# Kernel tuning notes

Hardware: AMD Instinct MI355X
Metric: run time of the kernel (lower is better)

Reference implementation:

```python
import jax, jax.numpy as jnp
import numpy as np

DECAY = 0.95     # importance_decay
BUDGET = 1.0     # attention_budget
TOP_K = 10       # recall top_k used by get_context_embedding
EPS = 1e-8


def _gelu(x):
    # torch nn.GELU default = exact erf variant
    return jax.nn.gelu(x, approximate=False)


def setup_inputs() -> dict:
    key = jax.random.key(0)
    ks = jax.random.split(key, 8)
    B, N, D, H = 4096, 100, 4096, 128
    query = jax.random.normal(ks[0], (B, D), dtype=jnp.float32)
    seg_emb = jax.random.normal(ks[1], (N, D), dtype=jnp.float32)
    positions = jnp.arange(N, dtype=jnp.int32)
    s1 = 1.0 / np.sqrt(D)
    s2 = 1.0 / np.sqrt(H)
    iw1 = jax.random.normal(ks[2], (D, H), dtype=jnp.float32) * s1
    ib1 = jnp.zeros((H,), dtype=jnp.float32)
    iw2 = jax.random.normal(ks[3], (H, 1), dtype=jnp.float32) * s2
    ib2 = jnp.zeros((1,), dtype=jnp.float32)
    rw1 = jax.random.normal(ks[4], (2 * D, H), dtype=jnp.float32) * (1.0 / np.sqrt(2 * D))
    rb1 = jnp.zeros((H,), dtype=jnp.float32)
    rw2 = jax.random.normal(ks[5], (H, 1), dtype=jnp.float32) * s2
    rb2 = jnp.zeros((1,), dtype=jnp.float32)
    return {"query": query, "seg_emb": seg_emb, "positions": positions,
            "iw1": iw1, "ib1": ib1, "iw2": iw2, "ib2": ib2,
            "rw1": rw1, "rb1": rb1, "rw2": rw2, "rb2": rb2}


def reference(query, seg_emb, positions, iw1, ib1, iw2, ib2, rw1, rb1, rw2, rb2):
    # query: [B, D], seg_emb: [N, D]
    B, D = query.shape
    N = seg_emb.shape[0]

    # importance_scorer per segment: Linear->GELU->Linear->Sigmoid, [N]
    importance = jax.nn.sigmoid(_gelu(seg_emb @ iw1 + ib1) @ iw2 + ib2)[:, 0]

    # relevance_scorer on concat([query, seg]); split rw1 to avoid [B,N,2D] concat
    qh = query @ rw1[:D]            # [B, H]
    sh = seg_emb @ rw1[D:]          # [N, H]
    h = _gelu(qh[:, None, :] + sh[None, :, :] + rb1)   # [B, N, H]
    rel = jax.nn.sigmoid(jnp.einsum('bnh,ho->bn', h, rw2) + rb2[0])  # [B, N]

    # recall score: importance * relevance * (0.5 + 0.5 * decay^(N - pos - 1))
    pos_factor = DECAY ** (N - positions.astype(jnp.float32) - 1.0)  # [N]
    score = importance[None, :] * rel * (0.5 + 0.5 * pos_factor[None, :])

    _, topi = jax.lax.top_k(score, TOP_K)               # [B, K]

    sel_rel = jnp.take_along_axis(rel, topi, axis=1)    # [B, K]
    sel_imp = importance[topi]                          # [B, K]
    w = sel_imp * sel_rel
    w = w / (jnp.sum(w, axis=-1, keepdims=True) + EPS) * BUDGET

    sel_emb = seg_emb[topi]                             # [B, K, D]
    context = jnp.einsum('bk,bkd->bd', w, sel_emb)      # [B, D]
    return query + context
```

## Files before the change

kernel.cpp:

```cpp
#include <hip/hip_runtime.h>
#include <math.h>

#define DDIM 4096
#define NSEG 100
#define HDIM 128
#define BROWS 4096
#define TOPK 10
#define KSLICES 8

typedef __attribute__((ext_vector_type(8))) short bf16x8;
typedef __attribute__((ext_vector_type(4))) float f32x4;
typedef __attribute__((ext_vector_type(2))) float f32x2;

__device__ __forceinline__ void gl16(const void* g, void* l) {
    __builtin_amdgcn_global_load_lds(
        (const __attribute__((address_space(1))) unsigned int*)g,
        (__attribute__((address_space(3))) unsigned int*)l,
        16, 0, 0);
}

__device__ __forceinline__ float gelu_f(float x) {
    float u  = x * 0.70710678118654752440f;
    float au = fminf(fabsf(u), 3.9f);
    float t  = __builtin_amdgcn_rcpf(fmaf(0.3275911f, au, 1.0f));
    float p  = fmaf(fmaf(fmaf(fmaf(1.061405429f, t, -1.453152027f), t,
                              1.421413741f), t, -0.284496736f), t, 0.254829592f) * t;
    float e  = __expf(-au * au);
    float er = fmaf(-p, e, 1.0f);
    er = copysignf(er, u);
    return 0.5f * x * (1.0f + er);
}

__device__ __forceinline__ f32x2 gelu2(f32x2 x) {
    f32x2 u  = x * 0.70710678118654752440f;
    f32x2 au = __builtin_elementwise_min(__builtin_elementwise_abs(u), (f32x2)(3.9f));
    f32x2 den = __builtin_elementwise_fma((f32x2)(0.3275911f), au, (f32x2)(1.0f));
    f32x2 t;
    t.x = __builtin_amdgcn_rcpf(den.x);
    t.y = __builtin_amdgcn_rcpf(den.y);
    f32x2 p = __builtin_elementwise_fma(
                __builtin_elementwise_fma(
                  __builtin_elementwise_fma(
                    __builtin_elementwise_fma((f32x2)(1.061405429f), t, (f32x2)(-1.453152027f)),
                    t, (f32x2)(1.421413741f)),
                  t, (f32x2)(-0.284496736f)),
                t, (f32x2)(0.254829592f)) * t;
    f32x2 e;
    e.x = __expf(-au.x * au.x);
    e.y = __expf(-au.y * au.y);
    f32x2 er = __builtin_elementwise_fma(-p, e, (f32x2)(1.0f));
    er.x = copysignf(er.x, u.x);
    er.y = copysignf(er.y, u.y);
    return 0.5f * x * ((f32x2)(1.0f) + er);
}

__device__ __forceinline__ void split8(const float4& a, const float4& b,
                                       bf16x8& hi, bf16x8& lo) {
    float v[8] = {a.x, a.y, a.z, a.w, b.x, b.y, b.z, b.w};
    uint hw[4], lw[4];
    #pragma unroll
    for (int j = 0; j < 4; ++j) {
        uint u0 = __float_as_uint(v[2 * j]);
        uint u1 = __float_as_uint(v[2 * j + 1]);
        hw[j] = (u0 >> 16) | (u1 & 0xffff0000u);
        float r0 = v[2 * j]     - __uint_as_float(u0 & 0xffff0000u);
        float r1 = v[2 * j + 1] - __uint_as_float(u1 & 0xffff0000u);
        lw[j] = (__float_as_uint(r0) >> 16) | (__float_as_uint(r1) & 0xffff0000u);
    }
    uint4 h = make_uint4(hw[0], hw[1], hw[2], hw[3]);
    uint4 l = make_uint4(lw[0], lw[1], lw[2], lw[3]);
    hi = __builtin_bit_cast(bf16x8, h);
    lo = __builtin_bit_cast(bf16x8, l);
}

__global__ void k_front(const float* __restrict__ seg,
                        const float* __restrict__ iw1,
                        const float* __restrict__ rw1,
                        float* __restrict__ segp,
                        unsigned char* __restrict__ btI) {
    __shared__ __align__(16) float shf[32 * 129];
    int bid = blockIdx.x, tid = threadIdx.x;
    if (bid < 1600) {
        float (*segT)[5] = reinterpret_cast<float (*)[5]>(shf);
        int ng = bid % 25;
        int ks = (bid / 25) * 64;
        {
            int k = tid & 63, j = tid >> 6;
            segT[k][j] = seg[(size_t)(ng * 4 + j) * DDIM + ks + k];
        }
        __syncthreads();
        int col = tid;
        float a0 = 0.f, a1 = 0.f, a2 = 0.f, a3 = 0.f;
        const float* w = (col < HDIM) ? (iw1 + col)
                                      : (rw1 + (size_t)DDIM * HDIM + (col - HDIM));
        #pragma unroll 8
        for (int k = 0; k < 64; ++k) {
            float wv = w[(size_t)(ks + k) * HDIM];
            a0 = fmaf(segT[k][0], wv, a0);
            a1 = fmaf(segT[k][1], wv, a1);
            a2 = fmaf(segT[k][2], wv, a2);
            a3 = fmaf(segT[k][3], wv, a3);
        }
        float* outp = segp + (size_t)(bid / 25) * (NSEG * 256) + (size_t)(ng * 4) * 256 + col;
        outp[0] = a0; outp[256] = a1; outp[512] = a2; outp[768] = a3;
    } else {
        float (*tile)[129] = reinterpret_cast<float (*)[129]>(shf);
        int c = bid - 1600;
        #pragma unroll
        for (int i = 0; i < 4; ++i) {
            int e = i * 1024 + tid * 4;
            int k = e >> 7, n = e & 127;
            *reinterpret_cast<float4*>(&tile[k][n]) =
                *reinterpret_cast<const float4*>(rw1 + (size_t)(c * 32 + k) * HDIM + n);
        }
        __syncthreads();
        unsigned char* img = btI + (size_t)c * 16384;
        #pragma unroll
        for (int uu = 0; uu < 2; ++uu) {
            int U = tid * 2 + uu;
            int col = U >> 2;
            int u = U & 3;
            int Z = (col * 64 + u * 16) ^ ((col & 7) << 4);
            uint hw[4], lw[4];
            #pragma unroll
            for (int j = 0; j < 4; ++j) {
                float x0 = tile[u * 8 + 2 * j][col];
                float x1 = tile[u * 8 + 2 * j + 1][col];
                uint u0 = __float_as_uint(x0), u1 = __float_as_uint(x1);
                hw[j] = (u0 >> 16) | (u1 & 0xffff0000u);
                float r0 = x0 - __uint_as_float(u0 & 0xffff0000u);
                float r1 = x1 - __uint_as_float(u1 & 0xffff0000u);
                lw[j] = (__float_as_uint(r0) >> 16) | (__float_as_uint(r1) & 0xffff0000u);
            }
            *reinterpret_cast<uint4*>(img + Z)        = make_uint4(hw[0], hw[1], hw[2], hw[3]);
            *reinterpret_cast<uint4*>(img + 8192 + Z) = make_uint4(lw[0], lw[1], lw[2], lw[3]);
        }
    }
}

__global__ __launch_bounds__(256)
void k_mid(const float* __restrict__ query,
           const unsigned char* __restrict__ btI,
           float* __restrict__ qhp,
           const float* __restrict__ segp,
           const int* __restrict__ positions,
           const float* __restrict__ ib1,
           const float* __restrict__ iw2,
           const float* __restrict__ ib2,
           const float* __restrict__ rb1,
           float* __restrict__ shwT, float* __restrict__ impA,
           float* __restrict__ cA) {
    __shared__ __align__(16) char lds[49152];
    int bid = blockIdx.x, tid = threadIdx.x;
    if (bid < 512) {
        float  (*Ab)[2048] = reinterpret_cast<float (*)[2048]>(lds);
        ushort (*Bb)[8192] = reinterpret_cast<ushort (*)[8192]>(lds + 16384);
        int lane = tid & 63, w = tid >> 6;
        int cl = lane & 15, rg = lane >> 4;
        int wm = w >> 1, wn = w & 1;
        int m0 = (bid & 63) * 64;
        int ky = bid >> 6;
        int k0 = ky * 512;

        const float* aSrc0;
        const float* aSrc1;
        {
            int X0 = w * 2048 + lane * 16;
            int r0_ = X0 >> 7, kb0 = (X0 & 127) ^ ((r0_ & 7) << 4);
            aSrc0 = query + (size_t)(m0 + r0_) * DDIM + k0 + (kb0 >> 2);
            int X1 = X0 + 1024;
            int r1_ = X1 >> 7, kb1 = (X1 & 127) ^ ((r1_ & 7) << 4);
            aSrc1 = query + (size_t)(m0 + r1_) * DDIM + k0 + (kb1 >> 2);
        }
        const unsigned char* bSrc = btI + (size_t)(ky * 16) * 16384 + w * 4096 + lane * 16;

        f32x4 acc[2][4];
        #pragma unroll
        for (int mi = 0; mi < 2; ++mi)
            #pragma unroll
            for (int nf = 0; nf < 4; ++nf) acc[mi][nf] = (f32x4)0.f;

        {
            char* ad = (char*)&Ab[0][0] + w * 2048;
            char* bd = (char*)&Bb[0][0] + w * 4096;
            gl16(aSrc0, ad);
            gl16(aSrc1, ad + 1024);
            #pragma unroll
            for (int j = 0; j < 4; ++j) gl16(bSrc + j * 1024, bd + j * 1024);
        }
        __syncthreads();

        #pragma unroll 2
        for (int t = 0; t < 16; ++t) {
            int cur = t & 1;
            if (t < 15) {
                char* ad = (char*)&Ab[cur ^ 1][0] + w * 2048;
                char* bd = (char*)&Bb[cur ^ 1][0] + w * 4096;
                gl16(aSrc0 + (t + 1) * 32, ad);
                gl16(aSrc1 + (t + 1) * 32, ad + 1024);
                const unsigned char* bs = bSrc + (size_t)(t + 1) * 16384;
                #pragma unroll
                for (int j = 0; j < 4; ++j) gl16(bs + j * 1024, bd + j * 1024);
            }
            bf16x8 ah[2], al[2];
            #pragma unroll
            for (int mi = 0; mi < 2; ++mi) {
                int row = wm * 32 + mi * 16 + cl;
                int sw = (row & 7) << 4;
                int Sb = row * 128 + rg * 32;
                float4 f0 = *reinterpret_cast<const float4*>((const char*)&Ab[cur][0] + (Sb ^ sw));
                float4 f1 = *reinterpret_cast<const float4*>((const char*)&Ab[cur][0] + ((Sb + 16) ^ sw));
                split8(f0, f1, ah[mi], al[mi]);
            }
            #pragma unroll
            for (int nf = 0; nf < 4; ++nf) {
                int col = wn * 64 + nf * 16 + cl;
                int Z = (col * 64 + rg * 16) ^ ((col & 7) << 4);
                bf16x8 bh = *reinterpret_cast<const bf16x8*>((const char*)&Bb[cur][0] + Z);
                bf16x8 bl = *reinterpret_cast<const bf16x8*>((const char*)&Bb[cur][0] + 8192 + Z);
                #pragma unroll
                for (int mi = 0; mi < 2; ++mi) {
                    acc[mi][nf] = __builtin_amdgcn_mfma_f32_16x16x32_bf16(ah[mi], bh, acc[mi][nf], 0, 0, 0);
                    acc[mi][nf] = __builtin_amdgcn_mfma_f32_16x16x32_bf16(al[mi], bh, acc[mi][nf], 0, 0, 0);
                    acc[mi][nf] = __builtin_amdgcn_mfma_f32_16x16x32_bf16(ah[mi], bl, acc[mi][nf], 0, 0, 0);
                }
            }
            __syncthreads();
        }

        float* op = qhp + (size_t)ky * (BROWS * HDIM);
        #pragma unroll
        for (int mi = 0; mi < 2; ++mi) {
            int rowb = m0 + wm * 32 + mi * 16 + rg * 4;
            #pragma unroll
            for (int nf = 0; nf < 4; ++nf) {
                int col = wn * 64 + nf * 16 + cl;
                #pragma unroll
                for (int r = 0; r < 4; ++r)
                    op[(size_t)(rowb + r) * HDIM + col] = acc[mi][nf][r];
            }
        }
    } else {
        float* red = reinterpret_cast<float*>(lds);
        int n = bid - 512;
        float v = 0.f;
        #pragma unroll
        for (int s = 0; s < 64; ++s)
            v += segp[(size_t)s * (NSEG * 256) + (size_t)n * 256 + tid];
        if (tid < HDIM) {
            red[tid] = gelu_f(v + ib1[tid]) * iw2[tid];
        } else {
            shwT[(size_t)(tid - HDIM) * NSEG + n] = v + rb1[tid - HDIM];
        }
        __syncthreads();
        if (tid == 0) {
            float s = 0.f;
            for (int j = 0; j < HDIM; ++j) s += red[j];
            float imp = 1.f / (1.f + expf(-(s + ib2[0])));
            float pf = powf(0.95f, (float)NSEG - (float)positions[n] - 1.0f);
            impA[n] = imp;
            cA[n] = imp * (0.5f + 0.5f * pf);
        }
    }
}

__global__ __launch_bounds__(256)
void k_rel(const float* __restrict__ qhp,
           const float* __restrict__ shwT,
           const float* __restrict__ rw2,
           const float* __restrict__ rb2,
           const float* __restrict__ impA,
           const float* __restrict__ cA,
           int* __restrict__ idxA,
           float* __restrict__ wnA) {
    __shared__ float qs[2][HDIM];
    __shared__ f32x2 part[2][2][64];
    __shared__ float scL[2][128], wiL[2][128];
    int tid = threadIdx.x;
    int b0 = blockIdx.x * 2;

    {
        int r = tid >> 7, h = tid & 127;
        size_t o = (size_t)(b0 + r) * HDIM + h;
        float v = qhp[o];
        #pragma unroll
        for (int s = 1; s < KSLICES; ++s)
            v += qhp[(size_t)s * (BROWS * HDIM) + o];
        qs[r][h] = v;
    }
    __syncthreads();

    int w = tid >> 6, lane = tid & 63;
    int rw_ = w & 1, hh = w >> 1;
    bool act = (lane < 50);
    int n0 = act ? (2 * lane) : 98;
    int hbase = hh * 64;
    f32x2 acc = (f32x2)(0.f);
    #pragma unroll 2
    for (int h = 0; h < 64; ++h) {
        int hz = hbase + h;
        f32x2 s2 = *reinterpret_cast<const f32x2*>(&shwT[hz * NSEG + n0]);
        float q = qs[rw_][hz];
        float wh = rw2[hz];
        acc = __builtin_elementwise_fma(gelu2(q + s2), (f32x2)(wh), acc);
    }
    part[rw_][hh][lane] = acc;
    __syncthreads();

    if (w < 2 && act) {
        f32x2 a = part[w][0][lane] + part[w][1][lane];
        float rb2f = rb2[0];
        float rel0 = 1.f / (1.f + expf(-(a.x + rb2f)));
        float rel1 = 1.f / (1.f + expf(-(a.y + rb2f)));
        scL[w][n0]     = cA[n0] * rel0;      wiL[w][n0]     = impA[n0] * rel0;
        scL[w][n0 + 1] = cA[n0 + 1] * rel1;  wiL[w][n0 + 1] = impA[n0 + 1] * rel1;
    }
    __syncthreads();

    if (w < 2) {
        int rr = w;
        float s1 = scL[rr][lane];
        float w1 = wiL[rr][lane];
        int i2 = lane + 64;
        float s2 = (i2 < NSEG) ? scL[rr][i2] : -1e30f;
        float w2 = (i2 < NSEG) ? wiL[rr][i2] : 0.f;

        float wv[TOPK]; int idxv[TOPK]; float wsum = 0.f;
        #pragma unroll
        for (int k = 0; k < TOPK; ++k) {
            float s; int i;
            if (s2 > s1) { s = s2; i = i2; } else { s = s1; i = lane; }
            #pragma unroll
            for (int off = 1; off < 64; off <<= 1) {
                float os = __shfl_xor(s, off);
                int oi = __shfl_xor(i, off);
                if (os > s || (os == s && oi < i)) { s = os; i = oi; }
            }
            float wi = __shfl((i < 64) ? w1 : w2, i & 63);
            idxv[k] = i; wv[k] = wi; wsum += wi;
            if (i == lane) s1 = -1e30f;
            if (i == i2)   s2 = -1e30f;
        }
        if (lane == 0) {
            int b = b0 + rr;
            float denom = wsum + 1e-8f;
            #pragma unroll
            for (int k = 0; k < TOPK; ++k) {
                idxA[b * TOPK + k] = idxv[k];
                wnA[b * TOPK + k]  = wv[k] / denom;
            }
        }
    }
}

__global__ void k_gather(const float* __restrict__ query,
                         const float* __restrict__ seg,
                         const int* __restrict__ idxA,
                         const float* __restrict__ wnA,
                         float* __restrict__ out) {
    int b = blockIdx.x, tid = threadIdx.x;
    const int*   ip = idxA + b * TOPK;
    const float* wp = wnA  + b * TOPK;
    float wn[TOPK]; const float* srow[TOPK];
    #pragma unroll
    for (int k = 0; k < TOPK; ++k) {
        wn[k]   = wp[k];
        srow[k] = seg + (size_t)ip[k] * DDIM;
    }
    const float* qrow = query + (size_t)b * DDIM;
    float* orow = out + (size_t)b * DDIM;

    float4 q[4];
    #pragma unroll
    for (int c = 0; c < 4; ++c)
        q[c] = *reinterpret_cast<const float4*>(qrow + c * 1024 + tid * 4);
    #pragma unroll
    for (int k = 0; k < TOPK; ++k) {
        float4 s[4];
        #pragma unroll
        for (int c = 0; c < 4; ++c)
            s[c] = *reinterpret_cast<const float4*>(srow[k] + c * 1024 + tid * 4);
        #pragma unroll
        for (int c = 0; c < 4; ++c) {
            q[c].x = fmaf(wn[k], s[c].x, q[c].x);
            q[c].y = fmaf(wn[k], s[c].y, q[c].y);
            q[c].z = fmaf(wn[k], s[c].z, q[c].z);
            q[c].w = fmaf(wn[k], s[c].w, q[c].w);
        }
    }
    #pragma unroll
    for (int c = 0; c < 4; ++c)
        *reinterpret_cast<float4*>(orow + c * 1024 + tid * 4) = q[c];
}

extern "C" void kernel_launch(void* const* d_in, const int* in_sizes, int n_in,
                              void* d_out, int out_size, void* d_ws, size_t ws_size,
                              hipStream_t stream) {
    const float* query = (const float*)d_in[0];
    const float* seg   = (const float*)d_in[1];
    const int*   pos   = (const int*)d_in[2];
    const float* iw1   = (const float*)d_in[3];
    const float* ib1   = (const float*)d_in[4];
    const float* iw2   = (const float*)d_in[5];
    const float* ib2   = (const float*)d_in[6];
    const float* rw1   = (const float*)d_in[7];
    const float* rb1   = (const float*)d_in[8];
    const float* rw2   = (const float*)d_in[9];
    const float* rb2   = (const float*)d_in[10];
    float* out = (float*)d_out;

    char* ws = (char*)d_ws;
    float* qhp  = (float*)(ws);
    float* segp = (float*)(ws + 16 * 1024 * 1024);
    unsigned char* btI = (unsigned char*)(ws + 23 * 1024 * 1024);
    float* shwT = (float*)(ws + 25 * 1024 * 1024);
    float* impA = (float*)(ws + 25 * 1024 * 1024 + 64 * 1024);
    float* cA   = (float*)(ws + 25 * 1024 * 1024 + 64 * 1024 + 4096);
    int*   idxA = (int*)  (ws + 25 * 1024 * 1024 + 128 * 1024);
    float* wnA  = (float*)(ws + 25 * 1024 * 1024 + 320 * 1024);

    hipLaunchKernelGGL(k_front, dim3(1728), dim3(256), 0, stream,
                       seg, iw1, rw1, segp, btI);
    hipLaunchKernelGGL(k_mid, dim3(612), dim3(256), 0, stream,
                       query, btI, qhp, segp, pos, ib1, iw2, ib2, rb1,
                       shwT, impA, cA);
    hipLaunchKernelGGL(k_rel, dim3(BROWS / 2), dim3(256), 0, stream,
                       qhp, shwT, rw2, rb2, impA, cA, idxA, wnA);
    hipLaunchKernelGGL(k_gather, dim3(BROWS), dim3(256), 0, stream,
                       query, seg, idxA, wnA, out);
}
```

Baseline: 115.7 us.

## Overlap second-half relevance scoring with first-half gather via split heterogeneous kernel

Splits the relevance/top-k kernel and the gather kernel into halves over the batch. A middle launch interleaves relevance blocks for rows 2048+ with gather blocks for rows 0-2047, whose indices come from the preceding launch. The aim is to overlap the compute-bound scoring with the memory-bound gather and cut tail idle time, at the cost of one extra launch and some branch divergence between block types.

```diff
diff --git a/kernel.cpp b/kernel.cpp
--- a/kernel.cpp
+++ b/kernel.cpp
@@ -264,20 +264,16 @@
     }
 }
 
-__global__ __launch_bounds__(256)
-void k_rel(const float* __restrict__ qhp,
-           const float* __restrict__ shwT,
-           const float* __restrict__ rw2,
-           const float* __restrict__ rb2,
-           const float* __restrict__ impA,
-           const float* __restrict__ cA,
-           int* __restrict__ idxA,
-           float* __restrict__ wnA) {
+__device__ __forceinline__ void rel2_body(
+        int b0,
+        const float* __restrict__ qhp, const float* __restrict__ shwT,
+        const float* __restrict__ rw2, const float* __restrict__ rb2,
+        const float* __restrict__ impA, const float* __restrict__ cA,
+        int* __restrict__ idxA, float* __restrict__ wnA) {
     __shared__ float qs[2][HDIM];
     __shared__ f32x2 part[2][2][64];
     __shared__ float scL[2][128], wiL[2][128];
     int tid = threadIdx.x;
-    int b0 = blockIdx.x * 2;
 
     {
         int r = tid >> 7, h = tid & 127;
@@ -353,12 +349,12 @@
     }
 }
 
-__global__ void k_gather(const float* __restrict__ query,
-                         const float* __restrict__ seg,
-                         const int* __restrict__ idxA,
-                         const float* __restrict__ wnA,
-                         float* __restrict__ out) {
-    int b = blockIdx.x, tid = threadIdx.x;
+__device__ __forceinline__ void gather_body(
+        int b,
+        const float* __restrict__ query, const float* __restrict__ seg,
+        const int* __restrict__ idxA, const float* __restrict__ wnA,
+        float* __restrict__ out) {
+    int tid = threadIdx.x;
     const int*   ip = idxA + b * TOPK;
     const float* wp = wnA  + b * TOPK;
     float wn[TOPK]; const float* srow[TOPK];
@@ -391,6 +387,37 @@
     #pragma unroll
     for (int c = 0; c < 4; ++c)
         *reinterpret_cast<float4*>(orow + c * 1024 + tid * 4) = q[c];
+}
+
+__global__ __launch_bounds__(256)
+void k_relA(const float* __restrict__ qhp, const float* __restrict__ shwT,
+            const float* __restrict__ rw2, const float* __restrict__ rb2,
+            const float* __restrict__ impA, const float* __restrict__ cA,
+            int* __restrict__ idxA, float* __restrict__ wnA) {
+    rel2_body(blockIdx.x * 2, qhp, shwT, rw2, rb2, impA, cA, idxA, wnA);
+}
+
+__global__ __launch_bounds__(256)
+void k_relgather(const float* __restrict__ qhp, const float* __restrict__ shwT,
+                 const float* __restrict__ rw2, const float* __restrict__ rb2,
+                 const float* __restrict__ impA, const float* __restrict__ cA,
+                 int* __restrict__ idxA, float* __restrict__ wnA,
+                 const float* __restrict__ query, const float* __restrict__ seg,
+                 float* __restrict__ out) {
+    int bid = blockIdx.x;
+    int m = bid % 3, g = bid / 3;
+    if (m == 0) {
+        rel2_body(2048 + g * 2, qhp, shwT, rw2, rb2, impA, cA, idxA, wnA);
+    } else {
+        gather_body(g * 2 + (m - 1), query, seg, idxA, wnA, out);
+    }
+}
+
+__global__ __launch_bounds__(256)
+void k_gatherB(const float* __restrict__ query, const float* __restrict__ seg,
+               const int* __restrict__ idxA, const float* __restrict__ wnA,
+               float* __restrict__ out) {
+    gather_body(2048 + blockIdx.x, query, seg, idxA, wnA, out);
 }
 
 extern "C" void kernel_launch(void* const* d_in, const int* in_sizes, int n_in,
@@ -424,8 +451,10 @@
     hipLaunchKernelGGL(k_mid, dim3(612), dim3(256), 0, stream,
                        query, btI, qhp, segp, pos, ib1, iw2, ib2, rb1,
                        shwT, impA, cA);
-    hipLaunchKernelGGL(k_rel, dim3(BROWS / 2), dim3(256), 0, stream,
+    hipLaunchKernelGGL(k_relA, dim3(1024), dim3(256), 0, stream,
                        qhp, shwT, rw2, rb2, impA, cA, idxA, wnA);
-    hipLaunchKernelGGL(k_gather, dim3(BROWS), dim3(256), 0, stream,
+    hipLaunchKernelGGL(k_relgather, dim3(3072), dim3(256), 0, stream,
+                       qhp, shwT, rw2, rb2, impA, cA, idxA, wnA, query, seg, out);
+    hipLaunchKernelGGL(k_gatherB, dim3(2048), dim3(256), 0, stream,
                        query, seg, idxA, wnA, out);
 }
```

Measured after the change: 127.4 us. 10.2% more time.
